# Kernel optimization log

Hardware: AMD Instinct MI355X
Metric: run time of the kernel (lower is better)

The kernel has to match this reference:

```python
import jax, jax.numpy as jnp
import numpy as np

N = 50000        # nodes
E = 800000       # edges (before self-loops)
F_IN = 256       # n_features
HID = 32         # hidden_dims (per-head out channels)
HEADS = 4
HC = HID * HEADS # 128, per-layer width
CLASSES = 40
LAYERS = 2
SLOPE = 0.1      # negative_slope for leaky_relu in attention


def _glorot(key, shape):
    fan_in, fan_out = shape[-2], shape[-1]
    lim = np.sqrt(6.0 / (fan_in + fan_out))
    return jax.random.uniform(key, shape, jnp.float32, -lim, lim)


def setup_inputs() -> dict:
    key = jax.random.key(0)
    ks = jax.random.split(key, 7)
    x = jax.random.normal(ks[0], (N, F_IN), jnp.float32)
    edge_index = jax.random.randint(ks[1], (2, E), 0, N, jnp.int64)
    weight_in = _glorot(ks[2], (F_IN, HC))
    weight_out = _glorot(ks[3], (HC, CLASSES))
    Ws = _glorot(ks[4], (LAYERS, HC, HC))            # per-layer GATConv linear
    atts = _glorot(ks[5], (LAYERS, HEADS, 2 * HID))  # [a_src | a_dst] per head
    biases = jnp.zeros((LAYERS, HC), jnp.float32)
    return {"x": x, "edge_index": edge_index, "weight_in": weight_in,
            "Ws": Ws, "atts": atts, "biases": biases, "weight_out": weight_out}


def _gat_conv(h, src, dst, W, att, bias):
    # h: [N, HC]; src/dst: [E'] edge endpoints (message src -> dst)
    n = h.shape[0]
    hp = (h @ W).reshape(n, HEADS, HID)                       # [N, H, C]
    a_src, a_dst = att[:, :HID], att[:, HID:]                 # [H, C] each
    alpha_src = jnp.einsum('nhc,hc->nh', hp, a_src)           # [N, H]
    alpha_dst = jnp.einsum('nhc,hc->nh', hp, a_dst)
    logits = jax.nn.leaky_relu(alpha_src[src] + alpha_dst[dst], SLOPE)  # [E', H]
    # softmax over edges grouped by destination node
    m = jax.ops.segment_max(logits, dst, num_segments=n)      # [N, H]
    e = jnp.exp(logits - m[dst])
    z = jax.ops.segment_sum(e, dst, num_segments=n)           # [N, H]
    alpha = e / z[dst]                                        # [E', H]
    msg = hp[src] * alpha[:, :, None]                         # [E', H, C]
    out = jax.ops.segment_sum(msg, dst, num_segments=n)       # [N, H, C]
    return out.reshape(n, HC) + bias


def reference(x, edge_index, weight_in, Ws, atts, biases, weight_out):
    # add self-loops (PyG GATConv default)
    loop = jnp.arange(N, dtype=edge_index.dtype)
    src = jnp.concatenate([edge_index[0], loop])
    dst = jnp.concatenate([edge_index[1], loop])
    h = x @ weight_in
    for l in range(LAYERS):
        # dropout is identity in eval mode
        h = jax.nn.elu(_gat_conv(h, src, dst, Ws[l], atts[l], biases[l]))
    return jax.nn.log_softmax(h @ weight_out, axis=1)
```

## Files before the change

kernel.cpp:

```cpp
#include <hip/hip_runtime.h>
#include <hip/hip_bf16.h>
#include <math.h>

#define N_NODES 50000
#define N_EDGES 800000
#define F_IN 256
#define HID 32
#define HEADS 4
#define HC 128
#define CLASSES 40
#define LAYERS 2
#define SLOPE 0.1f
#define EE (N_EDGES + N_NODES)

#define BSHIFT 9
#define NBUCK 98
#define BCAP 16384
#define CHUNK 4096
#define NBLK_E ((EE + CHUNK - 1) / CHUNK)
#define GEMM_BLOCKS ((N_NODES + 63) / 64)

typedef unsigned short ushortT;
typedef unsigned int uintT;
typedef __attribute__((ext_vector_type(8))) short short8v;
typedef __attribute__((ext_vector_type(4))) float f32x4;

__device__ __forceinline__ ushortT f2bu(float f) {
    __hip_bfloat16 h = __float2bfloat16(f);
    ushortT u; __builtin_memcpy(&u, &h, 2); return u;
}

__global__ void wconv_all(const float* __restrict__ w_in, const float* __restrict__ Ws,
                          const float* __restrict__ w_out, ushortT* __restrict__ w_inT,
                          ushortT* __restrict__ WsT, ushortT* __restrict__ woutT,
                          int* __restrict__ gcur) {
    int i = blockIdx.x * 256 + threadIdx.x;
    if (i < NBUCK) gcur[i] = 0;
    if (i < 32768) {
        int r = i >> 7, c = i & 127;
        w_inT[(size_t)c * F_IN + r] = f2bu(w_in[i]);
    } else if (i < 65536) {
        int j = i - 32768;
        int l = j >> 14, jj = j & 16383;
        int r = jj >> 7, c = jj & 127;
        WsT[l * 16384 + c * 128 + r] = f2bu(Ws[j]);
    } else if (i < 65536 + 6144) {
        int j = i - 65536;
        int c = j >> 7, k = j & 127;
        woutT[j] = (c < CLASSES) ? f2bu(w_out[k * CLASSES + c]) : (ushortT)0;
    }
}

#define AS_LD 40
template<bool AF32>
__device__ __forceinline__ void gemm_body(ushortT* As, ushortT* Bs,
                                          const void* __restrict__ Aptr,
                                          const ushortT* __restrict__ BT,
                                          ushortT* __restrict__ Cb,
                                          const float* __restrict__ att,
                                          float* __restrict__ asrc,
                                          float* __restrict__ adst,
                                          int M, int K, int bid) {
    int t = threadIdx.x;
    int w = t >> 6, lane = t & 63;
    int row0 = bid * 64;
    int ar = t >> 2, ak = (t & 3) * 8;
    int bcol = t >> 1, bks = (t & 1) * 16;
    int wr = w * 16;
    int arow = wr + (lane & 15);
    int ak8 = (lane >> 4) * 8;
    f32x4 acc[8] = {};

    for (int k0 = 0; k0 < K; k0 += 32) {
        int grow = row0 + ar;
        if (AF32) {
            const float* A = (const float*)Aptr;
            float4 v0 = make_float4(0.f, 0.f, 0.f, 0.f), v1 = v0;
            if (grow < M) {
                const float* ap = A + (size_t)grow * K + k0 + ak;
                v0 = *(const float4*)ap;
                v1 = *(const float4*)(ap + 4);
            }
            uint4 p;
            p.x = (uintT)f2bu(v0.x) | ((uintT)f2bu(v0.y) << 16);
            p.y = (uintT)f2bu(v0.z) | ((uintT)f2bu(v0.w) << 16);
            p.z = (uintT)f2bu(v1.x) | ((uintT)f2bu(v1.y) << 16);
            p.w = (uintT)f2bu(v1.z) | ((uintT)f2bu(v1.w) << 16);
            *(uint4*)&As[ar * AS_LD + ak] = p;
        } else {
            const ushortT* A = (const ushortT*)Aptr;
            uint4 p = make_uint4(0, 0, 0, 0);
            if (grow < M) p = *(const uint4*)(A + (size_t)grow * K + k0 + ak);
            *(uint4*)&As[ar * AS_LD + ak] = p;
        }
        {
            const ushortT* bp = BT + (size_t)bcol * K + k0 + bks;
            *(uint4*)&Bs[bcol * AS_LD + bks]     = *(const uint4*)bp;
            *(uint4*)&Bs[bcol * AS_LD + bks + 8] = *(const uint4*)(bp + 8);
        }
        __syncthreads();
        short8v a = *(short8v*)&As[arow * AS_LD + ak8];
#pragma unroll
        for (int c = 0; c < 8; ++c) {
            short8v b = *(short8v*)&Bs[(c * 16 + (lane & 15)) * AS_LD + ak8];
            acc[c] = __builtin_amdgcn_mfma_f32_16x16x32_bf16(a, b, acc[c], 0, 0, 0);
        }
        __syncthreads();
    }
    int cl = lane & 15;
    int r0 = row0 + wr + ((lane >> 4) << 2);
#pragma unroll
    for (int c = 0; c < 8; ++c) {
        int cc = c * 16 + cl;
#pragma unroll
        for (int r = 0; r < 4; ++r) {
            int rr = r0 + r;
            if (rr < M) Cb[(size_t)rr * 128 + cc] = f2bu(acc[c][r]);
        }
    }
    if (att) {
#pragma unroll
        for (int h = 0; h < HEADS; ++h) {
            float as0 = att[h * 64 + cl];
            float as1 = att[h * 64 + 16 + cl];
            float ad0 = att[h * 64 + 32 + cl];
            float ad1 = att[h * 64 + 48 + cl];
#pragma unroll
            for (int r = 0; r < 4; ++r) {
                float ps = acc[2 * h][r] * as0 + acc[2 * h + 1][r] * as1;
                float pd = acc[2 * h][r] * ad0 + acc[2 * h + 1][r] * ad1;
#pragma unroll
                for (int off = 1; off < 16; off <<= 1) {
                    ps += __shfl_xor(ps, off);
                    pd += __shfl_xor(pd, off);
                }
                int rr = r0 + r;
                if (cl == 0 && rr < M) {
                    asrc[rr * 4 + h] = ps;
                    adst[rr * 4 + h] = pd;
                }
            }
        }
    }
}

template<bool AF32>
__global__ __launch_bounds__(256) void gemm_mfma(const void* __restrict__ Aptr,
                                                 const ushortT* __restrict__ BT,
                                                 ushortT* __restrict__ Cb,
                                                 const float* __restrict__ att,
                                                 float* __restrict__ asrc,
                                                 float* __restrict__ adst,
                                                 int M, int K) {
    __shared__ ushortT As[64 * AS_LD];
    __shared__ ushortT Bs[128 * AS_LD];
    gemm_body<AF32>(As, Bs, Aptr, BT, Cb, att, asrc, adst, M, K, blockIdx.x);
}

__global__ __launch_bounds__(256) void gemm0_scatter(const float* __restrict__ x,
                                                     const ushortT* __restrict__ w_inT,
                                                     ushortT* __restrict__ hb0,
                                                     const int* __restrict__ ei,
                                                     int* __restrict__ gcur,
                                                     uintT* __restrict__ ebuf) {
    __shared__ ushortT As[64 * AS_LD];
    __shared__ ushortT Bs[128 * AS_LD];
    __shared__ int hist[NBUCK];
    __shared__ int rbase[NBUCK];
    if (blockIdx.x < GEMM_BLOCKS) {
        gemm_body<true>(As, Bs, x, w_inT, hb0, nullptr, nullptr, nullptr,
                        N_NODES, F_IN, blockIdx.x);
    } else {
        int t = threadIdx.x;
        if (t < NBUCK) hist[t] = 0;
        __syncthreads();
        int base = (blockIdx.x - GEMM_BLOCKS) * CHUNK;
        int end = min(base + CHUNK, EE);
        for (int i = base + t; i < end; i += 256) {
            int d = (i < N_EDGES) ? ei[N_EDGES + i] : (i - N_EDGES);
            atomicAdd(&hist[d >> BSHIFT], 1);
        }
        __syncthreads();
        if (t < NBUCK) {
            int c = hist[t];
            rbase[t] = c ? (t * BCAP + atomicAdd(&gcur[t], c)) : 0;
        }
        __syncthreads();
        if (t < NBUCK) hist[t] = 0;
        __syncthreads();
        for (int i = base + t; i < end; i += 256) {
            int s, d;
            if (i < N_EDGES) { s = ei[i]; d = ei[N_EDGES + i]; } else { s = d = i - N_EDGES; }
            int b = d >> BSHIFT;
            int pos = rbase[b] + atomicAdd(&hist[b], 1);
            ebuf[pos] = ((uintT)s << BSHIFT) | (uintT)(d & 511);
        }
    }
}

__device__ __forceinline__ void csr_local_body(const uintT* __restrict__ ebuf,
                                               const int* __restrict__ gcur,
                                               int2* __restrict__ rowinfo,
                                               int* __restrict__ ssrc, int b,
                                               int* cnt, int* cur, int* wsum) {
    int t = threadIdx.x;
    int node0 = b << BSHIFT;
    int nb = min(512, N_NODES - node0);
    int beg = b * BCAP;
    int end = beg + gcur[b];
    cnt[t] = 0; cnt[t + 256] = 0;
    __syncthreads();
    for (int i = beg + t; i < end; i += 256)
        atomicAdd(&cnt[ebuf[i] & 511], 1);
    __syncthreads();
    int v0 = cnt[2 * t], v1 = cnt[2 * t + 1];
    int s = v0 + v1;
    int lane = t & 63, w = t >> 6;
    int x = s;
#pragma unroll
    for (int off = 1; off < 64; off <<= 1) { int y = __shfl_up(x, off); if (lane >= off) x += y; }
    if (lane == 63) wsum[w] = x;
    __syncthreads();
    if (t == 0) { int run = 0; for (int k = 0; k < 4; ++k) { int tmp = wsum[k]; wsum[k] = run; run += tmp; } }
    __syncthreads();
    int excl = wsum[w] + x - s;
    cnt[2 * t] = excl; cnt[2 * t + 1] = excl + v0;
    cur[2 * t] = excl; cur[2 * t + 1] = excl + v0;
    if (2 * t < nb)     rowinfo[node0 + 2 * t]     = make_int2(beg + excl, v0);
    if (2 * t + 1 < nb) rowinfo[node0 + 2 * t + 1] = make_int2(beg + excl + v0, v1);
    __syncthreads();
    for (int i = beg + t; i < end; i += 256) {
        uintT e = ebuf[i];
        int pos = beg + atomicAdd(&cur[e & 511], 1);
        ssrc[pos] = (int)(e >> BSHIFT);
    }
}

__global__ __launch_bounds__(256) void gemm_csr(const ushortT* __restrict__ hin,
                                                const ushortT* __restrict__ BT,
                                                ushortT* __restrict__ hpb,
                                                const float* __restrict__ att,
                                                float* __restrict__ asrc,
                                                float* __restrict__ adst,
                                                const uintT* __restrict__ ebuf,
                                                const int* __restrict__ gcur,
                                                int2* __restrict__ rowinfo,
                                                int* __restrict__ ssrc) {
    __shared__ ushortT As[64 * AS_LD];
    __shared__ ushortT Bs[128 * AS_LD];
    __shared__ int cnt[512];
    __shared__ int cur[512];
    __shared__ int wsum[4];
    if (blockIdx.x < GEMM_BLOCKS) {
        gemm_body<false>(As, Bs, hin, BT, hpb, att, asrc, adst,
                         N_NODES, HC, blockIdx.x);
    } else {
        csr_local_body(ebuf, gcur, rowinfo, ssrc, blockIdx.x - GEMM_BLOCKS,
                       cnt, cur, wsum);
    }
}

__global__ __launch_bounds__(256) void cls_mfma(const ushortT* __restrict__ A,
                                                const ushortT* __restrict__ BT,
                                                float* __restrict__ out, int M) {
    __shared__ ushortT As[64 * AS_LD];
    __shared__ ushortT Bs[48 * AS_LD];
    int t = threadIdx.x;
    int w = t >> 6, lane = t & 63;
    int row0 = blockIdx.x * 64;
    int ar = t >> 2, ak = (t & 3) * 8;
    int wr = w * 16;
    int arow = wr + (lane & 15);
    int ak8 = (lane >> 4) * 8;
    f32x4 acc[3] = {};

    for (int k0 = 0; k0 < 128; k0 += 32) {
        int grow = row0 + ar;
        uint4 p = make_uint4(0, 0, 0, 0);
        if (grow < M) p = *(const uint4*)(A + (size_t)grow * 128 + k0 + ak);
        *(uint4*)&As[ar * AS_LD + ak] = p;
        if (t < 96) {
            int bcol = t >> 1, bks = (t & 1) * 16;
            const ushortT* bp = BT + bcol * 128 + k0 + bks;
            *(uint4*)&Bs[bcol * AS_LD + bks]     = *(const uint4*)bp;
            *(uint4*)&Bs[bcol * AS_LD + bks + 8] = *(const uint4*)(bp + 8);
        }
        __syncthreads();
        short8v a = *(short8v*)&As[arow * AS_LD + ak8];
#pragma unroll
        for (int c = 0; c < 3; ++c) {
            short8v b = *(short8v*)&Bs[(c * 16 + (lane & 15)) * AS_LD + ak8];
            acc[c] = __builtin_amdgcn_mfma_f32_16x16x32_bf16(a, b, acc[c], 0, 0, 0);
        }
        __syncthreads();
    }
    int cl = lane & 15;
    int r0 = row0 + wr + ((lane >> 4) << 2);
#pragma unroll
    for (int r = 0; r < 4; ++r) {
        float v0 = acc[0][r], v1 = acc[1][r];
        float v2 = (cl < 8) ? acc[2][r] : -1e30f;
        float m = fmaxf(fmaxf(v0, v1), v2);
#pragma unroll
        for (int off = 1; off < 16; off <<= 1) m = fmaxf(m, __shfl_xor(m, off));
        float e = __expf(v0 - m) + __expf(v1 - m) + ((cl < 8) ? __expf(v2 - m) : 0.f);
#pragma unroll
        for (int off = 1; off < 16; off <<= 1) e += __shfl_xor(e, off);
        float ls = m + __logf(e);
        int rr = r0 + r;
        if (rr < M) {
            float* o = out + (size_t)rr * CLASSES;
            o[cl] = v0 - ls;
            o[16 + cl] = v1 - ls;
            if (cl < 8) o[32 + cl] = v2 - ls;
        }
    }
}

__device__ __forceinline__ float lrelu(float v) { return v > 0.f ? v : SLOPE * v; }

__device__ __forceinline__ void gat_one(
    int node, int beg, int deg, int lane,
    const int* __restrict__ ssrc, const float* __restrict__ asrc,
    const float* __restrict__ adst, const ushortT* __restrict__ hpb,
    const float* __restrict__ bias, ushortT* __restrict__ foutB,
    float* sexp, int* ssrcl, float* sm)
{
    float4 ad = *(const float4*)(adst + (size_t)node * 4);
    int g = lane >> 4, i0 = lane & 15;
    float acc0 = 0.f, acc1 = 0.f;
    float zinv;
    const ushortT* hrow = hpb + lane * 2;

    if (deg <= 64) {
        float4 lg = make_float4(-1e30f, -1e30f, -1e30f, -1e30f);
        int soff = 0;
        if (lane < deg) {
            int s = ssrc[beg + lane];
            float4 a = *(const float4*)(asrc + (size_t)s * 4);
            lg.x = lrelu(a.x + ad.x);
            lg.y = lrelu(a.y + ad.y);
            lg.z = lrelu(a.z + ad.z);
            lg.w = lrelu(a.w + ad.w);
            soff = s * HC;
        }
        ssrcl[lane] = soff;
        *(float4*)&sexp[lane * 4] = lg;
        asm volatile("s_waitcnt lgkmcnt(0)" ::: "memory");
        float mg =     sexp[i0 * 4 + g];
        mg = fmaxf(mg, sexp[(i0 + 16) * 4 + g]);
        mg = fmaxf(mg, sexp[(i0 + 32) * 4 + g]);
        mg = fmaxf(mg, sexp[(i0 + 48) * 4 + g]);
#pragma unroll
        for (int off = 1; off < 16; off <<= 1) mg = fmaxf(mg, __shfl_xor(mg, off));
        if (i0 == 0) sm[g] = mg;
        asm volatile("s_waitcnt lgkmcnt(0)" ::: "memory");
        float4 m = *(float4*)&sm[0];
        float4 ex;
        ex.x = __expf(lg.x - m.x);
        ex.y = __expf(lg.y - m.y);
        ex.z = __expf(lg.z - m.z);
        ex.w = __expf(lg.w - m.w);
        *(float4*)&sexp[lane * 4] = ex;
        asm volatile("s_waitcnt lgkmcnt(0)" ::: "memory");
        float zg = sexp[i0 * 4 + g];
        zg +=      sexp[(i0 + 16) * 4 + g];
        zg +=      sexp[(i0 + 32) * 4 + g];
        zg +=      sexp[(i0 + 48) * 4 + g];
#pragma unroll
        for (int off = 1; off < 16; off <<= 1) zg += __shfl_xor(zg, off);
        zinv = 1.f / zg;
#pragma unroll 4
        for (int i = 0; i < deg; ++i) {
            float e = sexp[i * 4 + g];
            int off = ssrcl[i];
            uintT u = *(const uintT*)(hrow + off);
            acc0 = fmaf(__uint_as_float(u << 16),         e, acc0);
            acc1 = fmaf(__uint_as_float(u & 0xffff0000u), e, acc1);
        }
    } else {
        float4 m = make_float4(-1e30f, -1e30f, -1e30f, -1e30f);
        for (int i = lane; i < deg; i += 64) {
            int s = ssrc[beg + i];
            float4 a = *(const float4*)(asrc + (size_t)s * 4);
            m.x = fmaxf(m.x, lrelu(a.x + ad.x));
            m.y = fmaxf(m.y, lrelu(a.y + ad.y));
            m.z = fmaxf(m.z, lrelu(a.z + ad.z));
            m.w = fmaxf(m.w, lrelu(a.w + ad.w));
        }
#pragma unroll
        for (int off = 1; off < 64; off <<= 1) {
            m.x = fmaxf(m.x, __shfl_xor(m.x, off));
            m.y = fmaxf(m.y, __shfl_xor(m.y, off));
            m.z = fmaxf(m.z, __shfl_xor(m.z, off));
            m.w = fmaxf(m.w, __shfl_xor(m.w, off));
        }
        float4 zp = make_float4(0.f, 0.f, 0.f, 0.f);
        for (int c0 = 0; c0 < deg; c0 += 64) {
            int n_ch = min(64, deg - c0);
            if (lane < n_ch) {
                int s = ssrc[beg + c0 + lane];
                float4 a = *(const float4*)(asrc + (size_t)s * 4);
                float4 ex;
                ex.x = __expf(lrelu(a.x + ad.x) - m.x);
                ex.y = __expf(lrelu(a.y + ad.y) - m.y);
                ex.z = __expf(lrelu(a.z + ad.z) - m.z);
                ex.w = __expf(lrelu(a.w + ad.w) - m.w);
                *(float4*)&sexp[lane * 4] = ex;
                ssrcl[lane] = s * HC;
                zp.x += ex.x; zp.y += ex.y; zp.z += ex.z; zp.w += ex.w;
            }
            asm volatile("s_waitcnt lgkmcnt(0)" ::: "memory");
#pragma unroll 4
            for (int i = 0; i < n_ch; ++i) {
                float e = sexp[i * 4 + g];
                int off = ssrcl[i];
                uintT u = *(const uintT*)(hrow + off);
                acc0 = fmaf(__uint_as_float(u << 16),         e, acc0);
                acc1 = fmaf(__uint_as_float(u & 0xffff0000u), e, acc1);
            }
        }
#pragma unroll
        for (int off = 1; off < 64; off <<= 1) {
            zp.x += __shfl_xor(zp.x, off);
            zp.y += __shfl_xor(zp.y, off);
            zp.z += __shfl_xor(zp.z, off);
            zp.w += __shfl_xor(zp.w, off);
        }
        float zh = (g == 0) ? zp.x : (g == 1) ? zp.y : (g == 2) ? zp.z : zp.w;
        zinv = 1.f / zh;
    }

    float b0 = bias[lane * 2], b1 = bias[lane * 2 + 1];
    float v0 = acc0 * zinv + b0; v0 = v0 > 0.f ? v0 : __expf(v0) - 1.f;
    float v1 = acc1 * zinv + b1; v1 = v1 > 0.f ? v1 : __expf(v1) - 1.f;
    *(uintT*)(foutB + (size_t)node * HC + lane * 2) =
        (uintT)f2bu(v0) | ((uintT)f2bu(v1) << 16);
}

#define WPB 4
__global__ __launch_bounds__(256) void gat_gather2(
    const int2* __restrict__ rowinfo, const int* __restrict__ ssrc,
    const float* __restrict__ asrc, const float* __restrict__ adst,
    const ushortT* __restrict__ hpb, const float* __restrict__ bias,
    ushortT* __restrict__ foutB)
{
    __shared__ __align__(16) float s_exp[WPB][64][4];
    __shared__ int   s_src[WPB][64];
    __shared__ __align__(16) float s_m[WPB][8];
    __shared__ __align__(16) float s_z[WPB][8];
    int w = threadIdx.x >> 6;
    int lane = threadIdx.x & 63;
    int widx = blockIdx.x * WPB + w;
    int n0 = widx * 2;
    if (n0 >= N_NODES) return;
    int2 ri0 = rowinfo[n0];
    int2 ri1 = rowinfo[n0 + 1];
    int beg0 = ri0.x, deg0 = ri0.y;
    int beg1 = ri1.x, deg1 = ri1.y;

    if (deg0 <= 32 && deg1 <= 32) {
        int half = lane >> 5;
        int ll = lane & 31;
        int nn = n0 + half;
        int mybeg = half ? beg1 : beg0;
        int mydeg = half ? deg1 : deg0;
        float4 ad = *(const float4*)(adst + (size_t)nn * 4);
        float4 lg = make_float4(-1e30f, -1e30f, -1e30f, -1e30f);
        int soff = 0;
        if (ll < mydeg) {
            int s = ssrc[mybeg + ll];
            float4 a = *(const float4*)(asrc + (size_t)s * 4);
            lg.x = lrelu(a.x + ad.x);
            lg.y = lrelu(a.y + ad.y);
            lg.z = lrelu(a.z + ad.z);
            lg.w = lrelu(a.w + ad.w);
            soff = s * HC;
        }
        s_src[w][lane] = soff;
        *(float4*)&s_exp[w][lane][0] = lg;
        asm volatile("s_waitcnt lgkmcnt(0)" ::: "memory");
        int grp = lane >> 3, gi = lane & 7;
        int gbase = (grp >> 2) << 5;
        int gh = grp & 3;
        float mg =     s_exp[w][gbase + gi][gh];
        mg = fmaxf(mg, s_exp[w][gbase + gi +  8][gh]);
        mg = fmaxf(mg, s_exp[w][gbase + gi + 16][gh]);
        mg = fmaxf(mg, s_exp[w][gbase + gi + 24][gh]);
        mg = fmaxf(mg, __shfl_xor(mg, 1));
        mg = fmaxf(mg, __shfl_xor(mg, 2));
        mg = fmaxf(mg, __shfl_xor(mg, 4));
        if (gi == 0) s_m[w][grp] = mg;
        asm volatile("s_waitcnt lgkmcnt(0)" ::: "memory");
        float4 m = *(float4*)&s_m[w][half * 4];
        float4 ex;
        ex.x = __expf(lg.x - m.x);
        ex.y = __expf(lg.y - m.y);
        ex.z = __expf(lg.z - m.z);
        ex.w = __expf(lg.w - m.w);
        *(float4*)&s_exp[w][lane][0] = ex;
        asm volatile("s_waitcnt lgkmcnt(0)" ::: "memory");
        float zg = s_exp[w][gbase + gi][gh];
        zg +=      s_exp[w][gbase + gi +  8][gh];
        zg +=      s_exp[w][gbase + gi + 16][gh];
        zg +=      s_exp[w][gbase + gi + 24][gh];
        zg += __shfl_xor(zg, 1);
        zg += __shfl_xor(zg, 2);
        zg += __shfl_xor(zg, 4);
        if (gi == 0) s_z[w][grp] = zg;
        asm volatile("s_waitcnt lgkmcnt(0)" ::: "memory");
        int hd = ll >> 3;
        float zinv = 1.f / s_z[w][half * 4 + hd];
        int maxdeg = max(deg0, deg1);
        int ebase = half << 5;
        const ushortT* hrow = hpb + ll * 4;
        float a0 = 0.f, a1 = 0.f, a2 = 0.f, a3 = 0.f;
#pragma unroll 4
        for (int i = 0; i < maxdeg; ++i) {
            float e = s_exp[w][ebase + i][hd];
            int off = s_src[w][ebase + i];
            uint2 u = *(const uint2*)(hrow + off);
            a0 = fmaf(__uint_as_float(u.x << 16),         e, a0);
            a1 = fmaf(__uint_as_float(u.x & 0xffff0000u), e, a1);
            a2 = fmaf(__uint_as_float(u.y << 16),         e, a2);
            a3 = fmaf(__uint_as_float(u.y & 0xffff0000u), e, a3);
        }
        const float* bp = bias + ll * 4;
        float v0 = a0 * zinv + bp[0]; v0 = v0 > 0.f ? v0 : __expf(v0) - 1.f;
        float v1 = a1 * zinv + bp[1]; v1 = v1 > 0.f ? v1 : __expf(v1) - 1.f;
        float v2 = a2 * zinv + bp[2]; v2 = v2 > 0.f ? v2 : __expf(v2) - 1.f;
        float v3 = a3 * zinv + bp[3]; v3 = v3 > 0.f ? v3 : __expf(v3) - 1.f;
        uint2 o;
        o.x = (uintT)f2bu(v0) | ((uintT)f2bu(v1) << 16);
        o.y = (uintT)f2bu(v2) | ((uintT)f2bu(v3) << 16);
        *(uint2*)(foutB + (size_t)nn * HC + ll * 4) = o;
    } else {
        gat_one(n0,     beg0, deg0, lane, ssrc, asrc, adst, hpb, bias, foutB,
                &s_exp[w][0][0], &s_src[w][0], &s_m[w][0]);
        gat_one(n0 + 1, beg1, deg1, lane, ssrc, asrc, adst, hpb, bias, foutB,
                &s_exp[w][0][0], &s_src[w][0], &s_m[w][0]);
    }
}

extern "C" void kernel_launch(void* const* d_in, const int* in_sizes, int n_in,
                              void* d_out, int out_size, void* d_ws, size_t ws_size,
                              hipStream_t stream) {
    const float* x      = (const float*)d_in[0];
    const int*   ei     = (const int*)d_in[1];
    const float* w_in   = (const float*)d_in[2];
    const float* Ws     = (const float*)d_in[3];
    const float* atts   = (const float*)d_in[4];
    const float* biases = (const float*)d_in[5];
    const float* w_out  = (const float*)d_in[6];
    float* out = (float*)d_out;

    char* wp = (char*)d_ws;
    ushortT* hb0 = (ushortT*)wp; wp += (size_t)N_NODES * HC * 2;
    ushortT* hb1 = (ushortT*)wp; wp += (size_t)N_NODES * HC * 2;
    ushortT* hpb = (ushortT*)wp; wp += (size_t)N_NODES * HC * 2;
    float* asrc  = (float*)wp;   wp += (size_t)N_NODES * HEADS * 4;
    float* adst  = (float*)wp;   wp += (size_t)N_NODES * HEADS * 4;
    int2* rowinfo = (int2*)wp;   wp += (size_t)N_NODES * 8;
    int* ssrc    = (int*)wp;     wp += (size_t)NBUCK * BCAP * 4;
    uintT* ebuf  = (uintT*)wp;   wp += (size_t)NBUCK * BCAP * 4;
    int* gcur    = (int*)wp;     wp += (size_t)(NBUCK + 4) * 4;
    ushortT* w_inT = (ushortT*)wp; wp += (size_t)HC * F_IN * 2;
    ushortT* WsT   = (ushortT*)wp; wp += (size_t)LAYERS * HC * HC * 2;
    ushortT* woutT = (ushortT*)wp; wp += (size_t)48 * HC * 2;

    wconv_all<<<(32768 + 32768 + 6144 + 255) / 256, 256, 0, stream>>>(
        w_in, Ws, w_out, w_inT, WsT, woutT, gcur);

    gemm0_scatter<<<GEMM_BLOCKS + NBLK_E, 256, 0, stream>>>(x, w_inT, hb0, ei, gcur, ebuf);

    gemm_csr<<<GEMM_BLOCKS + NBUCK, 256, 0, stream>>>(
        hb0, WsT, hpb, atts, asrc, adst, ebuf, gcur, rowinfo, ssrc);

    int g2blk = (N_NODES / 2 + WPB - 1) / WPB;
    gat_gather2<<<g2blk, 64 * WPB, 0, stream>>>(
        rowinfo, ssrc, asrc, adst, hpb, biases, hb1);

    gemm_mfma<false><<<GEMM_BLOCKS, 256, 0, stream>>>(
        hb1, WsT + (size_t)HC * HC, hpb, atts + (size_t)HEADS * 2 * HID,
        asrc, adst, N_NODES, HC);
    gat_gather2<<<g2blk, 64 * WPB, 0, stream>>>(
        rowinfo, ssrc, asrc, adst, hpb, biases + HC, hb0);

    cls_mfma<<<GEMM_BLOCKS, 256, 0, stream>>>(hb0, woutT, out, N_NODES);
}
```

Measured before the change: 152.0 us.

## Fuse classifier GEMM and log-softmax into final GAT gather kernel

Removes the separate cls_mfma launch and instead computes the 128x40 output projection and log-softmax inside the second gat_gather2, using the ELU outputs kept in LDS (fp32) rather than writing them to global memory as bf16 and reading them back. Each half-wave computes one node's 40 logits with scalar FMAs against bf16 weights read from global memory/cache. This saves one kernel launch and the hidden-state round-trip, but replaces MFMA matrix work with per-lane scalar dot products, adds LDS usage, and keeps more precision in the hidden state.

```diff
diff --git a/kernel.cpp b/kernel.cpp
--- a/kernel.cpp
+++ b/kernel.cpp
@@ -260,63 +260,6 @@
     }
 }
 
-__global__ __launch_bounds__(256) void cls_mfma(const ushortT* __restrict__ A,
-                                                const ushortT* __restrict__ BT,
-                                                float* __restrict__ out, int M) {
-    __shared__ ushortT As[64 * AS_LD];
-    __shared__ ushortT Bs[48 * AS_LD];
-    int t = threadIdx.x;
-    int w = t >> 6, lane = t & 63;
-    int row0 = blockIdx.x * 64;
-    int ar = t >> 2, ak = (t & 3) * 8;
-    int wr = w * 16;
-    int arow = wr + (lane & 15);
-    int ak8 = (lane >> 4) * 8;
-    f32x4 acc[3] = {};
-
-    for (int k0 = 0; k0 < 128; k0 += 32) {
-        int grow = row0 + ar;
-        uint4 p = make_uint4(0, 0, 0, 0);
-        if (grow < M) p = *(const uint4*)(A + (size_t)grow * 128 + k0 + ak);
-        *(uint4*)&As[ar * AS_LD + ak] = p;
-        if (t < 96) {
-            int bcol = t >> 1, bks = (t & 1) * 16;
-            const ushortT* bp = BT + bcol * 128 + k0 + bks;
-            *(uint4*)&Bs[bcol * AS_LD + bks]     = *(const uint4*)bp;
-            *(uint4*)&Bs[bcol * AS_LD + bks + 8] = *(const uint4*)(bp + 8);
-        }
-        __syncthreads();
-        short8v a = *(short8v*)&As[arow * AS_LD + ak8];
-#pragma unroll
-        for (int c = 0; c < 3; ++c) {
-            short8v b = *(short8v*)&Bs[(c * 16 + (lane & 15)) * AS_LD + ak8];
-            acc[c] = __builtin_amdgcn_mfma_f32_16x16x32_bf16(a, b, acc[c], 0, 0, 0);
-        }
-        __syncthreads();
-    }
-    int cl = lane & 15;
-    int r0 = row0 + wr + ((lane >> 4) << 2);
-#pragma unroll
-    for (int r = 0; r < 4; ++r) {
-        float v0 = acc[0][r], v1 = acc[1][r];
-        float v2 = (cl < 8) ? acc[2][r] : -1e30f;
-        float m = fmaxf(fmaxf(v0, v1), v2);
-#pragma unroll
-        for (int off = 1; off < 16; off <<= 1) m = fmaxf(m, __shfl_xor(m, off));
-        float e = __expf(v0 - m) + __expf(v1 - m) + ((cl < 8) ? __expf(v2 - m) : 0.f);
-#pragma unroll
-        for (int off = 1; off < 16; off <<= 1) e += __shfl_xor(e, off);
-        float ls = m + __logf(e);
-        int rr = r0 + r;
-        if (rr < M) {
-            float* o = out + (size_t)rr * CLASSES;
-            o[cl] = v0 - ls;
-            o[16 + cl] = v1 - ls;
-            if (cl < 8) o[32 + cl] = v2 - ls;
-        }
-    }
-}
-
 __device__ __forceinline__ float lrelu(float v) { return v > 0.f ? v : SLOPE * v; }
 
 __device__ __forceinline__ void gat_one(
@@ -324,7 +267,7 @@
     const int* __restrict__ ssrc, const float* __restrict__ asrc,
     const float* __restrict__ adst, const ushortT* __restrict__ hpb,
     const float* __restrict__ bias, ushortT* __restrict__ foutB,
-    float* sexp, int* ssrcl, float* sm)
+    float* sexp, int* ssrcl, float* sm, float* lds_h)
 {
     float4 ad = *(const float4*)(adst + (size_t)node * 4);
     int g = lane >> 4, i0 = lane & 15;
@@ -434,21 +377,29 @@
     float b0 = bias[lane * 2], b1 = bias[lane * 2 + 1];
     float v0 = acc0 * zinv + b0; v0 = v0 > 0.f ? v0 : __expf(v0) - 1.f;
     float v1 = acc1 * zinv + b1; v1 = v1 > 0.f ? v1 : __expf(v1) - 1.f;
-    *(uintT*)(foutB + (size_t)node * HC + lane * 2) =
-        (uintT)f2bu(v0) | ((uintT)f2bu(v1) << 16);
+    if (lds_h) {
+        lds_h[lane * 2]     = v0;
+        lds_h[lane * 2 + 1] = v1;
+    } else {
+        *(uintT*)(foutB + (size_t)node * HC + lane * 2) =
+            (uintT)f2bu(v0) | ((uintT)f2bu(v1) << 16);
+    }
 }
 
 #define WPB 4
+template<bool DOCLS>
 __global__ __launch_bounds__(256) void gat_gather2(
     const int2* __restrict__ rowinfo, const int* __restrict__ ssrc,
     const float* __restrict__ asrc, const float* __restrict__ adst,
     const ushortT* __restrict__ hpb, const float* __restrict__ bias,
-    ushortT* __restrict__ foutB)
+    ushortT* __restrict__ foutB, const ushortT* __restrict__ woutT,
+    float* __restrict__ out)
 {
     __shared__ __align__(16) float s_exp[WPB][64][4];
     __shared__ int   s_src[WPB][64];
     __shared__ __align__(16) float s_m[WPB][8];
     __shared__ __align__(16) float s_z[WPB][8];
+    __shared__ __align__(16) float s_h[WPB][2][HC];
     int w = threadIdx.x >> 6;
     int lane = threadIdx.x & 63;
     int widx = blockIdx.x * WPB + w;
@@ -458,11 +409,11 @@
     int2 ri1 = rowinfo[n0 + 1];
     int beg0 = ri0.x, deg0 = ri0.y;
     int beg1 = ri1.x, deg1 = ri1.y;
+    int half = lane >> 5;
+    int ll = lane & 31;
+    int nn = n0 + half;
 
     if (deg0 <= 32 && deg1 <= 32) {
-        int half = lane >> 5;
-        int ll = lane & 31;
-        int nn = n0 + half;
         int mybeg = half ? beg1 : beg0;
         int mydeg = half ? deg1 : deg0;
         float4 ad = *(const float4*)(adst + (size_t)nn * 4);
@@ -530,15 +481,69 @@
         float v1 = a1 * zinv + bp[1]; v1 = v1 > 0.f ? v1 : __expf(v1) - 1.f;
         float v2 = a2 * zinv + bp[2]; v2 = v2 > 0.f ? v2 : __expf(v2) - 1.f;
         float v3 = a3 * zinv + bp[3]; v3 = v3 > 0.f ? v3 : __expf(v3) - 1.f;
-        uint2 o;
-        o.x = (uintT)f2bu(v0) | ((uintT)f2bu(v1) << 16);
-        o.y = (uintT)f2bu(v2) | ((uintT)f2bu(v3) << 16);
-        *(uint2*)(foutB + (size_t)nn * HC + ll * 4) = o;
+        if (DOCLS) {
+            *(float4*)&s_h[w][half][ll * 4] = make_float4(v0, v1, v2, v3);
+        } else {
+            uint2 o;
+            o.x = (uintT)f2bu(v0) | ((uintT)f2bu(v1) << 16);
+            o.y = (uintT)f2bu(v2) | ((uintT)f2bu(v3) << 16);
+            *(uint2*)(foutB + (size_t)nn * HC + ll * 4) = o;
+        }
     } else {
         gat_one(n0,     beg0, deg0, lane, ssrc, asrc, adst, hpb, bias, foutB,
-                &s_exp[w][0][0], &s_src[w][0], &s_m[w][0]);
+                &s_exp[w][0][0], &s_src[w][0], &s_m[w][0],
+                DOCLS ? &s_h[w][0][0] : nullptr);
         gat_one(n0 + 1, beg1, deg1, lane, ssrc, asrc, adst, hpb, bias, foutB,
-                &s_exp[w][0][0], &s_src[w][0], &s_m[w][0]);
+                &s_exp[w][0][0], &s_src[w][0], &s_m[w][0],
+                DOCLS ? &s_h[w][1][0] : nullptr);
+    }
+
+    if (DOCLS) {
+        asm volatile("s_waitcnt lgkmcnt(0)" ::: "memory");
+        const float* hl = &s_h[w][half][0];
+        float c1 = 0.f, c2 = 0.f;
+        const ushortT* w1 = woutT + ll * HC;
+#pragma unroll
+        for (int k8 = 0; k8 < 16; ++k8) {
+            float4 h0 = *(const float4*)&hl[k8 * 8];
+            float4 h1 = *(const float4*)&hl[k8 * 8 + 4];
+            uint4 wv = *(const uint4*)(w1 + k8 * 8);
+            c1 = fmaf(__uint_as_float(wv.x << 16),         h0.x, c1);
+            c1 = fmaf(__uint_as_float(wv.x & 0xffff0000u), h0.y, c1);
+            c1 = fmaf(__uint_as_float(wv.y << 16),         h0.z, c1);
+            c1 = fmaf(__uint_as_float(wv.y & 0xffff0000u), h0.w, c1);
+            c1 = fmaf(__uint_as_float(wv.z << 16),         h1.x, c1);
+            c1 = fmaf(__uint_as_float(wv.z & 0xffff0000u), h1.y, c1);
+            c1 = fmaf(__uint_as_float(wv.w << 16),         h1.z, c1);
+            c1 = fmaf(__uint_as_float(wv.w & 0xffff0000u), h1.w, c1);
+        }
+        if (ll < 8) {
+            const ushortT* w2 = woutT + (32 + ll) * HC;
+#pragma unroll
+            for (int k8 = 0; k8 < 16; ++k8) {
+                float4 h0 = *(const float4*)&hl[k8 * 8];
+                float4 h1 = *(const float4*)&hl[k8 * 8 + 4];
+                uint4 wv = *(const uint4*)(w2 + k8 * 8);
+                c2 = fmaf(__uint_as_float(wv.x << 16),         h0.x, c2);
+                c2 = fmaf(__uint_as_float(wv.x & 0xffff0000u), h0.y, c2);
+                c2 = fmaf(__uint_as_float(wv.y << 16),         h0.z, c2);
+                c2 = fmaf(__uint_as_float(wv.y & 0xffff0000u), h0.w, c2);
+                c2 = fmaf(__uint_as_float(wv.z << 16),         h1.x, c2);
+                c2 = fmaf(__uint_as_float(wv.z & 0xffff0000u), h1.y, c2);
+                c2 = fmaf(__uint_as_float(wv.w << 16),         h1.z, c2);
+                c2 = fmaf(__uint_as_float(wv.w & 0xffff0000u), h1.w, c2);
+            }
+        }
+        float mx = (ll < 8) ? fmaxf(c1, c2) : c1;
+#pragma unroll
+        for (int off = 1; off < 32; off <<= 1) mx = fmaxf(mx, __shfl_xor(mx, off));
+        float e = __expf(c1 - mx) + ((ll < 8) ? __expf(c2 - mx) : 0.f);
+#pragma unroll
+        for (int off = 1; off < 32; off <<= 1) e += __shfl_xor(e, off);
+        float ls = mx + __logf(e);
+        float* o = out + (size_t)nn * CLASSES;
+        o[ll] = c1 - ls;
+        if (ll < 8) o[32 + ll] = c2 - ls;
     }
 }
 
@@ -577,14 +582,12 @@
         hb0, WsT, hpb, atts, asrc, adst, ebuf, gcur, rowinfo, ssrc);
 
     int g2blk = (N_NODES / 2 + WPB - 1) / WPB;
-    gat_gather2<<<g2blk, 64 * WPB, 0, stream>>>(
-        rowinfo, ssrc, asrc, adst, hpb, biases, hb1);
+    gat_gather2<false><<<g2blk, 64 * WPB, 0, stream>>>(
+        rowinfo, ssrc, asrc, adst, hpb, biases, hb1, nullptr, nullptr);
 
     gemm_mfma<false><<<GEMM_BLOCKS, 256, 0, stream>>>(
         hb1, WsT + (size_t)HC * HC, hpb, atts + (size_t)HEADS * 2 * HID,
         asrc, adst, N_NODES, HC);
-    gat_gather2<<<g2blk, 64 * WPB, 0, stream>>>(
-        rowinfo, ssrc, asrc, adst, hpb, biases + HC, hb0);
-
-    cls_mfma<<<GEMM_BLOCKS, 256, 0, stream>>>(hb0, woutT, out, N_NODES);
-}
+    gat_gather2<true><<<g2blk, 64 * WPB, 0, stream>>>(
+        rowinfo, ssrc, asrc, adst, hpb, biases + HC, nullptr, woutT, out);
+}
```

Result: slower. 240.4 us (+58.1%).
